# Kernel optimization log

Hardware: AMD Instinct MI355X
Metric: run time of the kernel (lower is better)

## Reference

```python
import jax, jax.numpy as jnp
import numpy as np

NUM_USERS = 500000
NUM_LAYERS = 3
AUDIO_SCALE = 1.0
METADATA_SCALE = 0.5
EPS = 1e-12


def _l2norm(x):
    # matches F.normalize(p=2, dim=-1, eps=1e-12): x / max(||x||, eps)
    n = jnp.sqrt(jnp.sum(x * x, axis=-1, keepdims=True))
    return x / jnp.maximum(n, EPS)


def setup_inputs() -> dict:
    key = jax.random.key(0)
    ks = jax.random.split(key, 12)
    N_SUB, E, D = 131072, 2097152, 64
    NUM_ITEMS, NUM_ARTISTS, NUM_ALBUMS = 500000, 50000, 100000
    batch_nodes = jax.random.randint(ks[0], (N_SUB,), 0, NUM_USERS + NUM_ITEMS, dtype=jnp.int64 if jax.config.jax_enable_x64 else jnp.int32)
    edge_index_sub = jax.random.randint(ks[1], (2, E), 0, N_SUB)
    edge_weight_init_sub = jax.random.uniform(ks[2], (E,), dtype=jnp.float32)
    user_emb_w = jax.random.normal(ks[3], (NUM_USERS, D), dtype=jnp.float32)
    artist_emb_w = jax.random.normal(ks[4], (NUM_ARTISTS, D), dtype=jnp.float32) * 0.05
    album_emb_w = jax.random.normal(ks[5], (NUM_ALBUMS, D), dtype=jnp.float32) * 0.05
    item_audio_emb = jax.random.normal(ks[6], (NUM_ITEMS, D), dtype=jnp.float32)
    artist_ids = jax.random.randint(ks[7], (NUM_ITEMS,), 0, NUM_ARTISTS)
    album_ids = jax.random.randint(ks[8], (NUM_ITEMS,), 0, NUM_ALBUMS)
    proj_w = jax.random.normal(ks[9], (2 * D, D), dtype=jnp.float32) * 0.05
    proj_b = jnp.zeros((D,), dtype=jnp.float32)
    return {
        'batch_nodes': batch_nodes,
        'edge_index_sub': edge_index_sub,
        'edge_weight_init_sub': edge_weight_init_sub,
        'user_emb_w': user_emb_w,
        'artist_emb_w': artist_emb_w,
        'album_emb_w': album_emb_w,
        'item_audio_emb': item_audio_emb,
        'artist_ids': artist_ids,
        'album_ids': album_ids,
        'proj_w': proj_w,
        'proj_b': proj_b,
    }


def reference(batch_nodes, edge_index_sub, edge_weight_init_sub,
              user_emb_w, artist_emb_w, album_emb_w, item_audio_emb,
              artist_ids, album_ids, proj_w, proj_b):
    N = batch_nodes.shape[0]
    row, col = edge_index_sub[0], edge_index_sub[1]

    # add_remaining_self_loops(fill_value=1.0): keep existing edges, append a
    # self-loop for every node; nodes that already have a self-loop get weight 0
    # for the appended loop (a zero-weight edge contributes nothing to deg or
    # aggregation, so this is mathematically identical to PyG's behavior).
    has_loop = jax.ops.segment_sum((row == col).astype(jnp.float32), row, num_segments=N) > 0
    loop_w = jnp.where(has_loop, 0.0, 1.0)
    ar = jnp.arange(N, dtype=row.dtype)
    row_f = jnp.concatenate([row, ar])
    col_f = jnp.concatenate([col, ar])
    w_f = jnp.concatenate([edge_weight_init_sub, loop_w])

    # gcn_norm: deg over targets, symmetric normalization
    deg = jax.ops.segment_sum(w_f, col_f, num_segments=N)
    dinv = jnp.where(deg > 0, jax.lax.rsqrt(jnp.maximum(deg, EPS)), 0.0)
    norm = dinv[row_f] * w_f * dinv[col_f]  # [E+N]

    # node features: users -> normalized user embedding; items -> projected
    user_mask = batch_nodes < NUM_USERS
    u_idx = jnp.where(user_mask, batch_nodes, 0)
    i_idx = jnp.where(user_mask, 0, batch_nodes - NUM_USERS)

    user_e = _l2norm(user_emb_w[u_idx])  # [N, D]
    audio_part = item_audio_emb[i_idx] * AUDIO_SCALE
    meta_part = (artist_emb_w[artist_ids[i_idx]] + album_emb_w[album_ids[i_idx]]) * METADATA_SCALE
    item_e = _l2norm(jnp.concatenate([audio_part, meta_part], axis=-1) @ proj_w + proj_b)

    x = jnp.where(user_mask[:, None], user_e, item_e)  # [N, D]

    # LightGCN propagation: mean over layer-0..num_layers embeddings
    acc = x
    for _ in range(NUM_LAYERS):
        msg = norm[:, None] * x[row_f]              # [E+N, D] gather
        x = jax.ops.segment_sum(msg, col_f, num_segments=N)  # scatter-add
        acc = acc + x
    out = _l2norm(acc / (NUM_LAYERS + 1))
    return out
```

## Files before the change

kernel.cpp:

```cpp
#include <hip/hip_runtime.h>

#define NUM_USERS_C 500000
#define EPS_F 1e-12f

__global__ void k_edgeprep(const int* __restrict__ row, const int* __restrict__ col,
                           const float* __restrict__ w,
                           int* __restrict__ flags, float* __restrict__ deg,
                           int* __restrict__ cnt, int E) {
    int e = blockIdx.x * blockDim.x + threadIdx.x;
    if (e < E) {
        int r = row[e], c = col[e];
        if (r == c) flags[r] = 1;
        atomicAdd(&deg[c], w[e]);
        atomicAdd(&cnt[c], 1);
    }
}

__global__ void k_dinv(const float* __restrict__ deg, const int* __restrict__ flags,
                       float* __restrict__ dinv, float* __restrict__ selfw, int N) {
    int n = blockIdx.x * blockDim.x + threadIdx.x;
    if (n < N) {
        float lw = flags[n] ? 0.0f : 1.0f;
        float d = deg[n] + lw;
        float di = (d > 0.0f) ? rsqrtf(fmaxf(d, EPS_F)) : 0.0f;
        dinv[n] = di;
        selfw[n] = di * di * lw;
    }
}

__global__ __launch_bounds__(256) void k_blocksum(const int* __restrict__ cnt,
                                                  int* __restrict__ bsum, int N) {
    __shared__ int s[256];
    int i = blockIdx.x * 256 + threadIdx.x;
    s[threadIdx.x] = (i < N) ? cnt[i] : 0;
    __syncthreads();
    for (int d = 128; d > 0; d >>= 1) {
        if (threadIdx.x < d) s[threadIdx.x] += s[threadIdx.x + d];
        __syncthreads();
    }
    if (threadIdx.x == 0) bsum[blockIdx.x] = s[0];
}

__global__ __launch_bounds__(1024) void k_scanbsum(const int* __restrict__ bsum,
                                                   int* __restrict__ boff,
                                                   int* __restrict__ rowptr,
                                                   int NB, int N) {
    __shared__ int s[1024];
    int t = threadIdx.x;
    int v = (t < NB) ? bsum[t] : 0;
    s[t] = v;
    __syncthreads();
    for (int d = 1; d < 1024; d <<= 1) {
        int u = (t >= d) ? s[t - d] : 0;
        __syncthreads();
        s[t] += u;
        __syncthreads();
    }
    if (t < NB) boff[t] = s[t] - v;
    if (t == 1023) rowptr[N] = s[1023];
}

__global__ __launch_bounds__(256) void k_rowptr(const int* __restrict__ cnt,
                                                const int* __restrict__ boff,
                                                int* __restrict__ rowptr, int N) {
    __shared__ int s[256];
    int i = blockIdx.x * 256 + threadIdx.x;
    int v = (i < N) ? cnt[i] : 0;
    s[threadIdx.x] = v;
    __syncthreads();
    for (int d = 1; d < 256; d <<= 1) {
        int u = (threadIdx.x >= d) ? s[threadIdx.x - d] : 0;
        __syncthreads();
        s[threadIdx.x] += u;
        __syncthreads();
    }
    if (i < N) rowptr[i] = boff[blockIdx.x] + s[threadIdx.x] - v;
}

__global__ void k_scatter(const int* __restrict__ row, const int* __restrict__ col,
                          const float* __restrict__ w, const float* __restrict__ dinv,
                          const int* __restrict__ rowptr, int* __restrict__ cursor,
                          int2* __restrict__ emeta, int E) {
    int e = blockIdx.x * blockDim.x + threadIdx.x;
    if (e < E) {
        int r = row[e], c = col[e];
        float nm = dinv[r] * w[e] * dinv[c];
        int pos = rowptr[c] + atomicAdd(&cursor[c], 1);
        emeta[pos] = make_int2(r, __float_as_int(nm));
    }
}

__global__ __launch_bounds__(256) void k_features(
    const int* __restrict__ batch_nodes,
    const float* __restrict__ user_emb, const float* __restrict__ artist_emb,
    const float* __restrict__ album_emb, const float* __restrict__ audio_emb,
    const int* __restrict__ artist_ids, const int* __restrict__ album_ids,
    const float* __restrict__ proj_w, const float* __restrict__ proj_b,
    float* __restrict__ x, float* __restrict__ acc, int N)
{
    __shared__ float Ws[128 * 64];
    for (int i = threadIdx.x; i < 128 * 64; i += blockDim.x)
        Ws[i] = proj_w[i];
    __syncthreads();

    const int lane = threadIdx.x & 63;
    const int wid = threadIdx.x >> 6;
    const int wavesPerBlock = blockDim.x >> 6;
    const int waveStride = gridDim.x * wavesPerBlock;
    const float bias = proj_b[lane];

    for (int n = blockIdx.x * wavesPerBlock + wid; n < N; n += waveStride) {
        int idx = batch_nodes[n];
        float val;
        if (idx < NUM_USERS_C) {
            val = user_emb[(size_t)idx * 64 + lane];
        } else {
            int it = idx - NUM_USERS_C;
            int aid = artist_ids[it];
            int bid = album_ids[it];
            float vlo = audio_emb[(size_t)it * 64 + lane];
            float vhi = 0.5f * (artist_emb[(size_t)aid * 64 + lane] +
                                album_emb[(size_t)bid * 64 + lane]);
            float s = bias;
            #pragma unroll
            for (int k = 0; k < 64; k++)
                s = fmaf(__shfl(vlo, k, 64), Ws[k * 64 + lane], s);
            #pragma unroll
            for (int k = 0; k < 64; k++)
                s = fmaf(__shfl(vhi, k, 64), Ws[(k + 64) * 64 + lane], s);
            val = s;
        }
        float ss = val * val;
        #pragma unroll
        for (int off = 32; off > 0; off >>= 1) ss += __shfl_xor(ss, off, 64);
        float scale = 1.0f / fmaxf(sqrtf(ss), EPS_F);
        val *= scale;
        x[(size_t)n * 64 + lane] = val;
        acc[(size_t)n * 64 + lane] = val;
    }
}

__device__ __forceinline__ float prop_accum(
    const int* __restrict__ rowptr, const int2* __restrict__ emeta,
    const float* __restrict__ selfw, const float* __restrict__ xs,
    int node, int lane)
{
    int beg = rowptr[node], end = rowptr[node + 1];
    float a = selfw[node] * xs[(size_t)node * 64 + lane];
    for (int base = beg; base < end; base += 64) {
        int chunk = min(64, end - base);
        int2 m = make_int2(0, 0);
        if (lane < chunk) m = emeta[base + lane];
        int j = 0;
        for (; j + 8 <= chunk; j += 8) {
            int r0 = __shfl(m.x, j + 0); float w0 = __int_as_float(__shfl(m.y, j + 0));
            int r1 = __shfl(m.x, j + 1); float w1 = __int_as_float(__shfl(m.y, j + 1));
            int r2 = __shfl(m.x, j + 2); float w2 = __int_as_float(__shfl(m.y, j + 2));
            int r3 = __shfl(m.x, j + 3); float w3 = __int_as_float(__shfl(m.y, j + 3));
            int r4 = __shfl(m.x, j + 4); float w4 = __int_as_float(__shfl(m.y, j + 4));
            int r5 = __shfl(m.x, j + 5); float w5 = __int_as_float(__shfl(m.y, j + 5));
            int r6 = __shfl(m.x, j + 6); float w6 = __int_as_float(__shfl(m.y, j + 6));
            int r7 = __shfl(m.x, j + 7); float w7 = __int_as_float(__shfl(m.y, j + 7));
            float v0 = xs[(size_t)r0 * 64 + lane];
            float v1 = xs[(size_t)r1 * 64 + lane];
            float v2 = xs[(size_t)r2 * 64 + lane];
            float v3 = xs[(size_t)r3 * 64 + lane];
            float v4 = xs[(size_t)r4 * 64 + lane];
            float v5 = xs[(size_t)r5 * 64 + lane];
            float v6 = xs[(size_t)r6 * 64 + lane];
            float v7 = xs[(size_t)r7 * 64 + lane];
            a = fmaf(w0, v0, a); a = fmaf(w1, v1, a);
            a = fmaf(w2, v2, a); a = fmaf(w3, v3, a);
            a = fmaf(w4, v4, a); a = fmaf(w5, v5, a);
            a = fmaf(w6, v6, a); a = fmaf(w7, v7, a);
        }
        for (; j < chunk; j++) {
            int r = __shfl(m.x, j); float wv = __int_as_float(__shfl(m.y, j));
            a = fmaf(wv, xs[(size_t)r * 64 + lane], a);
        }
    }
    return a;
}

__global__ __launch_bounds__(256) void k_prop(
    const int* __restrict__ rowptr, const int2* __restrict__ emeta,
    const float* __restrict__ selfw,
    const float* __restrict__ xs, float* __restrict__ xd,
    float* __restrict__ acc, int N)
{
    int lane = threadIdx.x & 63;
    int node = blockIdx.x * 4 + (threadIdx.x >> 6);
    if (node >= N) return;
    float a = prop_accum(rowptr, emeta, selfw, xs, node, lane);
    xd[(size_t)node * 64 + lane] = a;
    acc[(size_t)node * 64 + lane] += a;
}

__global__ __launch_bounds__(256) void k_prop_final(
    const int* __restrict__ rowptr, const int2* __restrict__ emeta,
    const float* __restrict__ selfw,
    const float* __restrict__ xs, float* __restrict__ acc_out, int N)
{
    int lane = threadIdx.x & 63;
    int node = blockIdx.x * 4 + (threadIdx.x >> 6);
    if (node >= N) return;
    float a = prop_accum(rowptr, emeta, selfw, xs, node, lane);
    float v = (acc_out[(size_t)node * 64 + lane] + a) * 0.25f;
    float ss = v * v;
    #pragma unroll
    for (int off = 32; off > 0; off >>= 1) ss += __shfl_xor(ss, off, 64);
    float scale = 1.0f / fmaxf(sqrtf(ss), EPS_F);
    acc_out[(size_t)node * 64 + lane] = v * scale;
}

extern "C" void kernel_launch(void* const* d_in, const int* in_sizes, int n_in,
                              void* d_out, int out_size, void* d_ws, size_t ws_size,
                              hipStream_t stream) {
    const int*   batch_nodes = (const int*)d_in[0];
    const int*   edge_index  = (const int*)d_in[1];
    const float* edge_w      = (const float*)d_in[2];
    const float* user_emb    = (const float*)d_in[3];
    const float* artist_emb  = (const float*)d_in[4];
    const float* album_emb   = (const float*)d_in[5];
    const float* audio_emb   = (const float*)d_in[6];
    const int*   artist_ids  = (const int*)d_in[7];
    const int*   album_ids   = (const int*)d_in[8];
    const float* proj_w      = (const float*)d_in[9];
    const float* proj_b      = (const float*)d_in[10];

    const int N = in_sizes[0];
    const int E = in_sizes[2];
    const int* row = edge_index;
    const int* col = edge_index + E;
    float* out = (float*)d_out;

    const int NB = (N + 255) / 256;

    char* ws = (char*)d_ws;
    float* deg    = (float*)ws; ws += (size_t)N * sizeof(float);
    float* dinv   = (float*)ws; ws += (size_t)N * sizeof(float);
    float* selfw  = (float*)ws; ws += (size_t)N * sizeof(float);
    int*   flags  = (int*)ws;   ws += (size_t)N * sizeof(int);
    int*   cnt    = (int*)ws;   ws += (size_t)N * sizeof(int);
    int*   cursor = (int*)ws;   ws += (size_t)N * sizeof(int);
    int*   rowptr = (int*)ws;   ws += (size_t)(N + 1) * sizeof(int);
    int*   bsum   = (int*)ws;   ws += (size_t)NB * sizeof(int);
    int*   boff   = (int*)ws;   ws += (size_t)NB * sizeof(int);
    ws = (char*)(((uintptr_t)ws + 15) & ~(uintptr_t)15);
    int2*  emeta  = (int2*)ws;  ws += (size_t)E * sizeof(int2);
    float* xA     = (float*)ws; ws += (size_t)N * 64 * sizeof(float);
    float* xB     = (float*)ws; ws += (size_t)N * 64 * sizeof(float);

    hipMemsetAsync(deg, 0, (size_t)N * sizeof(float), stream);
    hipMemsetAsync(flags, 0, (size_t)N * sizeof(int), stream);
    hipMemsetAsync(cnt, 0, (size_t)N * sizeof(int), stream);
    hipMemsetAsync(cursor, 0, (size_t)N * sizeof(int), stream);

    const int TB = 256;

    k_edgeprep<<<(E + TB - 1) / TB, TB, 0, stream>>>(row, col, edge_w, flags, deg, cnt, E);
    k_dinv<<<(N + TB - 1) / TB, TB, 0, stream>>>(deg, flags, dinv, selfw, N);
    k_blocksum<<<NB, 256, 0, stream>>>(cnt, bsum, N);
    k_scanbsum<<<1, 1024, 0, stream>>>(bsum, boff, rowptr, NB, N);
    k_rowptr<<<NB, 256, 0, stream>>>(cnt, boff, rowptr, N);
    k_scatter<<<(E + TB - 1) / TB, TB, 0, stream>>>(row, col, edge_w, dinv,
                                                    rowptr, cursor, emeta, E);

    k_features<<<4096, 256, 0, stream>>>(batch_nodes, user_emb, artist_emb, album_emb,
                                         audio_emb, artist_ids, album_ids, proj_w, proj_b,
                                         xA, out, N);

    int pblocks = (N + 3) / 4;
    k_prop<<<pblocks, 256, 0, stream>>>(rowptr, emeta, selfw, xA, xB, out, N);
    k_prop<<<pblocks, 256, 0, stream>>>(rowptr, emeta, selfw, xB, xA, out, N);
    k_prop_final<<<pblocks, 256, 0, stream>>>(rowptr, emeta, selfw, xA, out, N);
}
```

Baseline: 1.035 ms.

## Factor symmetric norm into per-node scaling and compute degree from CSR

Edge metadata now stores the raw edge weight. The symmetric normalization is factored into per-node dinv scaling applied before and after each propagation layer. Degree is computed by a per-node wave reduction over the CSR instead of float atomics. The first pass records each edge's slot, which removes the second atomic pass and the cursor buffer, and the feature projection uses readlane with four accumulators instead of shuffles. This trades E float atomics and E atomics in the scatter for an extra N-node CSR sweep, and adds a small change in floating-point rounding order.

```diff
diff --git a/kernel.cpp b/kernel.cpp
--- a/kernel.cpp
+++ b/kernel.cpp
@@ -4,27 +4,13 @@
 #define EPS_F 1e-12f
 
 __global__ void k_edgeprep(const int* __restrict__ row, const int* __restrict__ col,
-                           const float* __restrict__ w,
-                           int* __restrict__ flags, float* __restrict__ deg,
-                           int* __restrict__ cnt, int E) {
+                           int* __restrict__ flags, int* __restrict__ cnt,
+                           int* __restrict__ slot, int E) {
     int e = blockIdx.x * blockDim.x + threadIdx.x;
     if (e < E) {
         int r = row[e], c = col[e];
         if (r == c) flags[r] = 1;
-        atomicAdd(&deg[c], w[e]);
-        atomicAdd(&cnt[c], 1);
-    }
-}
-
-__global__ void k_dinv(const float* __restrict__ deg, const int* __restrict__ flags,
-                       float* __restrict__ dinv, float* __restrict__ selfw, int N) {
-    int n = blockIdx.x * blockDim.x + threadIdx.x;
-    if (n < N) {
-        float lw = flags[n] ? 0.0f : 1.0f;
-        float d = deg[n] + lw;
-        float di = (d > 0.0f) ? rsqrtf(fmaxf(d, EPS_F)) : 0.0f;
-        dinv[n] = di;
-        selfw[n] = di * di * lw;
+        slot[e] = atomicAdd(&cnt[c], 1);
     }
 }
 
@@ -78,16 +64,34 @@
 }
 
 __global__ void k_scatter(const int* __restrict__ row, const int* __restrict__ col,
-                          const float* __restrict__ w, const float* __restrict__ dinv,
-                          const int* __restrict__ rowptr, int* __restrict__ cursor,
+                          const float* __restrict__ w, const int* __restrict__ slot,
+                          const int* __restrict__ rowptr,
                           int2* __restrict__ emeta, int E) {
     int e = blockIdx.x * blockDim.x + threadIdx.x;
     if (e < E) {
-        int r = row[e], c = col[e];
-        float nm = dinv[r] * w[e] * dinv[c];
-        int pos = rowptr[c] + atomicAdd(&cursor[c], 1);
-        emeta[pos] = make_int2(r, __float_as_int(nm));
-    }
+        int c = col[e];
+        int pos = rowptr[c] + slot[e];
+        emeta[pos] = make_int2(row[e], __float_as_int(w[e]));
+    }
+}
+
+__global__ __launch_bounds__(256) void k_deg(const int* __restrict__ rowptr,
+                                             const int2* __restrict__ emeta,
+                                             const int* __restrict__ flags,
+                                             float2* __restrict__ dinfo, int N) {
+    int lane = threadIdx.x & 63;
+    int node = blockIdx.x * 4 + (threadIdx.x >> 6);
+    if (node >= N) return;
+    int beg = rowptr[node], end = rowptr[node + 1];
+    float s = 0.0f;
+    for (int i = beg + lane; i < end; i += 64)
+        s += __int_as_float(emeta[i].y);
+    #pragma unroll
+    for (int off = 32; off > 0; off >>= 1) s += __shfl_xor(s, off, 64);
+    float lw = flags[node] ? 0.0f : 1.0f;
+    float d = s + lw;
+    float di = (d > 0.0f) ? rsqrtf(fmaxf(d, EPS_F)) : 0.0f;
+    if (lane == 0) dinfo[node] = make_float2(di, lw);
 }
 
 __global__ __launch_bounds__(256) void k_features(
@@ -96,7 +100,8 @@
     const float* __restrict__ album_emb, const float* __restrict__ audio_emb,
     const int* __restrict__ artist_ids, const int* __restrict__ album_ids,
     const float* __restrict__ proj_w, const float* __restrict__ proj_b,
-    float* __restrict__ x, float* __restrict__ acc, int N)
+    const float2* __restrict__ dinfo,
+    float* __restrict__ xt, float* __restrict__ acc, int N)
 {
     __shared__ float Ws[128 * 64];
     for (int i = threadIdx.x; i < 128 * 64; i += blockDim.x)
@@ -121,32 +126,50 @@
             float vlo = audio_emb[(size_t)it * 64 + lane];
             float vhi = 0.5f * (artist_emb[(size_t)aid * 64 + lane] +
                                 album_emb[(size_t)bid * 64 + lane]);
-            float s = bias;
+            int ilo = __float_as_int(vlo);
+            int ihi = __float_as_int(vhi);
+            float s0 = bias, s1 = 0.0f, s2 = 0.0f, s3 = 0.0f;
             #pragma unroll
-            for (int k = 0; k < 64; k++)
-                s = fmaf(__shfl(vlo, k, 64), Ws[k * 64 + lane], s);
+            for (int k = 0; k < 64; k += 4) {
+                float a0 = __int_as_float(__builtin_amdgcn_readlane(ilo, k + 0));
+                float a1 = __int_as_float(__builtin_amdgcn_readlane(ilo, k + 1));
+                float a2 = __int_as_float(__builtin_amdgcn_readlane(ilo, k + 2));
+                float a3 = __int_as_float(__builtin_amdgcn_readlane(ilo, k + 3));
+                s0 = fmaf(a0, Ws[(k + 0) * 64 + lane], s0);
+                s1 = fmaf(a1, Ws[(k + 1) * 64 + lane], s1);
+                s2 = fmaf(a2, Ws[(k + 2) * 64 + lane], s2);
+                s3 = fmaf(a3, Ws[(k + 3) * 64 + lane], s3);
+            }
             #pragma unroll
-            for (int k = 0; k < 64; k++)
-                s = fmaf(__shfl(vhi, k, 64), Ws[(k + 64) * 64 + lane], s);
-            val = s;
+            for (int k = 0; k < 64; k += 4) {
+                float a0 = __int_as_float(__builtin_amdgcn_readlane(ihi, k + 0));
+                float a1 = __int_as_float(__builtin_amdgcn_readlane(ihi, k + 1));
+                float a2 = __int_as_float(__builtin_amdgcn_readlane(ihi, k + 2));
+                float a3 = __int_as_float(__builtin_amdgcn_readlane(ihi, k + 3));
+                s0 = fmaf(a0, Ws[(k + 64) * 64 + lane], s0);
+                s1 = fmaf(a1, Ws[(k + 65) * 64 + lane], s1);
+                s2 = fmaf(a2, Ws[(k + 66) * 64 + lane], s2);
+                s3 = fmaf(a3, Ws[(k + 67) * 64 + lane], s3);
+            }
+            val = (s0 + s1) + (s2 + s3);
         }
         float ss = val * val;
         #pragma unroll
         for (int off = 32; off > 0; off >>= 1) ss += __shfl_xor(ss, off, 64);
         float scale = 1.0f / fmaxf(sqrtf(ss), EPS_F);
         val *= scale;
-        x[(size_t)n * 64 + lane] = val;
+        float di = dinfo[n].x;
         acc[(size_t)n * 64 + lane] = val;
+        xt[(size_t)n * 64 + lane] = di * val;
     }
 }
 
 __device__ __forceinline__ float prop_accum(
     const int* __restrict__ rowptr, const int2* __restrict__ emeta,
-    const float* __restrict__ selfw, const float* __restrict__ xs,
-    int node, int lane)
+    const float* __restrict__ xs, int node, int lane, float lw)
 {
     int beg = rowptr[node], end = rowptr[node + 1];
-    float a = selfw[node] * xs[(size_t)node * 64 + lane];
+    float a = lw * xs[(size_t)node * 64 + lane];
     for (int base = beg; base < end; base += 64) {
         int chunk = min(64, end - base);
         int2 m = make_int2(0, 0);
@@ -184,28 +207,32 @@
 
 __global__ __launch_bounds__(256) void k_prop(
     const int* __restrict__ rowptr, const int2* __restrict__ emeta,
-    const float* __restrict__ selfw,
+    const float2* __restrict__ dinfo,
     const float* __restrict__ xs, float* __restrict__ xd,
     float* __restrict__ acc, int N)
 {
     int lane = threadIdx.x & 63;
     int node = blockIdx.x * 4 + (threadIdx.x >> 6);
     if (node >= N) return;
-    float a = prop_accum(rowptr, emeta, selfw, xs, node, lane);
-    xd[(size_t)node * 64 + lane] = a;
-    acc[(size_t)node * 64 + lane] += a;
+    float2 dn = dinfo[node];
+    float t = prop_accum(rowptr, emeta, xs, node, lane, dn.y);
+    float xnext = dn.x * t;
+    acc[(size_t)node * 64 + lane] += xnext;
+    xd[(size_t)node * 64 + lane] = dn.x * xnext;
 }
 
 __global__ __launch_bounds__(256) void k_prop_final(
     const int* __restrict__ rowptr, const int2* __restrict__ emeta,
-    const float* __restrict__ selfw,
+    const float2* __restrict__ dinfo,
     const float* __restrict__ xs, float* __restrict__ acc_out, int N)
 {
     int lane = threadIdx.x & 63;
     int node = blockIdx.x * 4 + (threadIdx.x >> 6);
     if (node >= N) return;
-    float a = prop_accum(rowptr, emeta, selfw, xs, node, lane);
-    float v = (acc_out[(size_t)node * 64 + lane] + a) * 0.25f;
+    float2 dn = dinfo[node];
+    float t = prop_accum(rowptr, emeta, xs, node, lane, dn.y);
+    float xnext = dn.x * t;
+    float v = (acc_out[(size_t)node * 64 + lane] + xnext) * 0.25f;
     float ss = v * v;
     #pragma unroll
     for (int off = 32; off > 0; off >>= 1) ss += __shfl_xor(ss, off, 64);
@@ -237,41 +264,38 @@
     const int NB = (N + 255) / 256;
 
     char* ws = (char*)d_ws;
-    float* deg    = (float*)ws; ws += (size_t)N * sizeof(float);
-    float* dinv   = (float*)ws; ws += (size_t)N * sizeof(float);
-    float* selfw  = (float*)ws; ws += (size_t)N * sizeof(float);
-    int*   flags  = (int*)ws;   ws += (size_t)N * sizeof(int);
-    int*   cnt    = (int*)ws;   ws += (size_t)N * sizeof(int);
-    int*   cursor = (int*)ws;   ws += (size_t)N * sizeof(int);
-    int*   rowptr = (int*)ws;   ws += (size_t)(N + 1) * sizeof(int);
-    int*   bsum   = (int*)ws;   ws += (size_t)NB * sizeof(int);
-    int*   boff   = (int*)ws;   ws += (size_t)NB * sizeof(int);
+    int*    flags  = (int*)ws;    ws += (size_t)N * sizeof(int);
+    int*    cnt    = (int*)ws;    ws += (size_t)N * sizeof(int);
+    int*    rowptr = (int*)ws;    ws += (size_t)(N + 1) * sizeof(int);
+    int*    bsum   = (int*)ws;    ws += (size_t)NB * sizeof(int);
+    int*    boff   = (int*)ws;    ws += (size_t)NB * sizeof(int);
     ws = (char*)(((uintptr_t)ws + 15) & ~(uintptr_t)15);
-    int2*  emeta  = (int2*)ws;  ws += (size_t)E * sizeof(int2);
-    float* xA     = (float*)ws; ws += (size_t)N * 64 * sizeof(float);
-    float* xB     = (float*)ws; ws += (size_t)N * 64 * sizeof(float);
-
-    hipMemsetAsync(deg, 0, (size_t)N * sizeof(float), stream);
+    float2* dinfo  = (float2*)ws; ws += (size_t)N * sizeof(float2);
+    int2*   emeta  = (int2*)ws;   ws += (size_t)E * sizeof(int2);
+    float*  xA     = (float*)ws;  ws += (size_t)N * 64 * sizeof(float);
+    float*  xB     = (float*)ws;  ws += (size_t)N * 64 * sizeof(float);
+    int*    slot   = (int*)xB;
+
     hipMemsetAsync(flags, 0, (size_t)N * sizeof(int), stream);
     hipMemsetAsync(cnt, 0, (size_t)N * sizeof(int), stream);
-    hipMemsetAsync(cursor, 0, (size_t)N * sizeof(int), stream);
 
     const int TB = 256;
 
-    k_edgeprep<<<(E + TB - 1) / TB, TB, 0, stream>>>(row, col, edge_w, flags, deg, cnt, E);
-    k_dinv<<<(N + TB - 1) / TB, TB, 0, stream>>>(deg, flags, dinv, selfw, N);
+    k_edgeprep<<<(E + TB - 1) / TB, TB, 0, stream>>>(row, col, flags, cnt, slot, E);
     k_blocksum<<<NB, 256, 0, stream>>>(cnt, bsum, N);
     k_scanbsum<<<1, 1024, 0, stream>>>(bsum, boff, rowptr, NB, N);
     k_rowptr<<<NB, 256, 0, stream>>>(cnt, boff, rowptr, N);
-    k_scatter<<<(E + TB - 1) / TB, TB, 0, stream>>>(row, col, edge_w, dinv,
-                                                    rowptr, cursor, emeta, E);
+    k_scatter<<<(E + TB - 1) / TB, TB, 0, stream>>>(row, col, edge_w, slot,
+                                                    rowptr, emeta, E);
+
+    int pblocks = (N + 3) / 4;
+    k_deg<<<pblocks, 256, 0, stream>>>(rowptr, emeta, flags, dinfo, N);
 
     k_features<<<4096, 256, 0, stream>>>(batch_nodes, user_emb, artist_emb, album_emb,
                                          audio_emb, artist_ids, album_ids, proj_w, proj_b,
-                                         xA, out, N);
-
-    int pblocks = (N + 3) / 4;
-    k_prop<<<pblocks, 256, 0, stream>>>(rowptr, emeta, selfw, xA, xB, out, N);
-    k_prop<<<pblocks, 256, 0, stream>>>(rowptr, emeta, selfw, xB, xA, out, N);
-    k_prop_final<<<pblocks, 256, 0, stream>>>(rowptr, emeta, selfw, xA, out, N);
-}
+                                         dinfo, xA, out, N);
+
+    k_prop<<<pblocks, 256, 0, stream>>>(rowptr, emeta, dinfo, xA, xB, out, N);
+    k_prop<<<pblocks, 256, 0, stream>>>(rowptr, emeta, dinfo, xB, xA, out, N);
+    k_prop_final<<<pblocks, 256, 0, stream>>>(rowptr, emeta, dinfo, xA, out, N);
+}
```

New measurement: 878.5 us. 15.1% less time.
